# Performance work log

Hardware: AMD Instinct MI355X
Metric: run time of the kernel (lower is better)

The kernel has to match this reference:

```python
import jax, jax.numpy as jnp
import numpy as np

B, C, H, W = 32, 256, 32, 32
C8 = C // 8


def setup_inputs() -> dict:
    key = jax.random.key(0)
    ks = jax.random.split(key, 8)
    s = 1.0 / np.sqrt(C)
    return {
        "x": jax.random.normal(ks[0], (B, C, H, W), dtype=jnp.float32),
        "Wq": jax.random.normal(ks[1], (C8, C), dtype=jnp.float32) * s,
        "bq": jax.random.normal(ks[2], (C8,), dtype=jnp.float32) * s,
        "Wk": jax.random.normal(ks[3], (C8, C), dtype=jnp.float32) * s,
        "bk": jax.random.normal(ks[4], (C8,), dtype=jnp.float32) * s,
        "Wv": jax.random.normal(ks[5], (C, C), dtype=jnp.float32) * s,
        "bv": jax.random.normal(ks[6], (C,), dtype=jnp.float32) * s,
        "gamma": jax.random.normal(ks[7], (1,), dtype=jnp.float32) * 0.1,
    }


def reference(x, Wq, bq, Wk, bk, Wv, bv, gamma):
    b, c, h, w = x.shape
    n = h * w
    xf = x.reshape(b, c, n)  # [B, C, N]
    # 1x1 convs == per-pixel linear projections
    q = jnp.einsum('dc,bcn->bnd', Wq, xf) + bq            # [B, N, C/8]
    k = jnp.einsum('dc,bcn->bdn', Wk, xf) + bk[:, None]    # [B, C/8, N]
    v = jnp.einsum('dc,bcn->bdn', Wv, xf) + bv[:, None]    # [B, C, N]
    energy = jnp.einsum('bnd,bdm->bnm', q, k)              # [B, N, N], no scaling (as in source)
    attn = jax.nn.softmax(energy, axis=-1)                 # softmax over keys
    # out[:, :, i] = sum_j V[:, :, j] * attn[i, j]
    out = jnp.einsum('bdn,bmn->bdm', v, attn)              # [B, C, N]
    out = out.reshape(b, c, h, w)
    return gamma * out + x
```

## Files before the change

kernel.cpp:

```cpp
#include <hip/hip_runtime.h>
#include <math.h>

#define BB 32
#define CC 256
#define CQ 32
#define NN 1024

typedef short bf16x8 __attribute__((ext_vector_type(8)));
typedef float f32x4  __attribute__((ext_vector_type(4)));
typedef unsigned short u16;

__device__ __forceinline__ u16 f2bf(float f) {
    unsigned u = __float_as_uint(f);
    u = (u + 0x7FFFu + ((u >> 16) & 1u)) >> 16;
    return (u16)u;
}

__device__ __forceinline__ unsigned cvt_pk_bf16(float lo, float hi) {
    unsigned r;
    asm("v_cvt_pk_bf16_f32 %0, %1, %2" : "=v"(r) : "v"(lo), "v"(hi));
    return r;
}

__global__ void wpack_kernel(const float* __restrict__ Wq,
                             const float* __restrict__ Wk,
                             const float* __restrict__ Wv,
                             u16* __restrict__ wfrag)
{
    const int o = blockIdx.x * 256 + threadIdx.x;
    const int j    = o & 7;
    const int lane = (o >> 3) & 63;
    const int kc   = (o >> 9) & 7;
    const int rt   = o >> 12;
    const int row  = rt * 16 + (lane & 15);
    const int col  = kc * 32 + (lane >> 4) * 8 + j;
    const float v = (row < 32) ? Wq[row * 256 + col]
                  : (row < 64) ? Wk[(row - 32) * 256 + col]
                               : Wv[(row - 64) * 256 + col];
    wfrag[o] = f2bf(v);
}

struct QSmem {
    union {
        u16 xs[32][268];
        u16 osv[CC][40];
    };
    u16 osqk[32][72];
};

__global__ __launch_bounds__(256, 4) void qkv_kernel(
    const float* __restrict__ x, const u16* __restrict__ wfrag,
    const float* __restrict__ bq, const float* __restrict__ bk,
    const float* __restrict__ bv,
    u16* __restrict__ qt, u16* __restrict__ kt, u16* __restrict__ vv)
{
    __shared__ QSmem sm;
    const int b = blockIdx.y, n0 = blockIdx.x * 32;
    const int t = threadIdx.x;
    const int lane = t & 63, w = t >> 6;
    const int quad = lane >> 4, c16 = lane & 15;

    {
        const float* xb = x + (size_t)b * CC * NN + n0;
        const int n4 = (t & 7) * 4;
        const int cr = t >> 3;
        float4 f[8];
#pragma unroll
        for (int it = 0; it < 8; ++it)
            f[it] = *(const float4*)(xb + (size_t)(it * 32 + cr) * NN + n4);
#pragma unroll
        for (int it = 0; it < 8; ++it) {
            const int c = it * 32 + cr;
            sm.xs[n4 + 0][c] = f2bf(f[it].x);
            sm.xs[n4 + 1][c] = f2bf(f[it].y);
            sm.xs[n4 + 2][c] = f2bf(f[it].z);
            sm.xs[n4 + 3][c] = f2bf(f[it].w);
        }
    }
    __syncthreads();

    f32x4 acc[5][2];
#pragma unroll
    for (int i = 0; i < 5; ++i)
#pragma unroll
        for (int j = 0; j < 2; ++j) acc[i][j] = (f32x4){0.f, 0.f, 0.f, 0.f};

#pragma unroll 2
    for (int k = 0; k < 8; ++k) {
        const int c0 = k * 32;
        bf16x8 wa[5], xb[2];
#pragma unroll
        for (int rs = 0; rs < 5; ++rs)
            wa[rs] = *(const bf16x8*)&wfrag[(size_t)(((w * 5 + rs) * 8 + k) * 64 + lane) * 8];
#pragma unroll
        for (int ns = 0; ns < 2; ++ns) {
            const short4 a = *(const short4*)&sm.xs[ns * 16 + c16][c0 + quad * 8];
            const short4 b2 = *(const short4*)&sm.xs[ns * 16 + c16][c0 + quad * 8 + 4];
            bf16x8 v;
            v[0] = a.x; v[1] = a.y; v[2] = a.z; v[3] = a.w;
            v[4] = b2.x; v[5] = b2.y; v[6] = b2.z; v[7] = b2.w;
            xb[ns] = v;
        }
#pragma unroll
        for (int rs = 0; rs < 5; ++rs)
#pragma unroll
            for (int ns = 0; ns < 2; ++ns)
                acc[rs][ns] = __builtin_amdgcn_mfma_f32_16x16x32_bf16(
                    wa[rs], xb[ns], acc[rs][ns], 0, 0, 0);
    }

    __syncthreads();

#pragma unroll
    for (int rs = 0; rs < 5; ++rs) {
#pragma unroll
        for (int r = 0; r < 4; ++r) {
            const int rg = w * 80 + rs * 16 + quad * 4 + r;
            const float bias = (rg < 32) ? bq[rg] : (rg < 64) ? bk[rg - 32] : bv[rg - 64];
#pragma unroll
            for (int ns = 0; ns < 2; ++ns) {
                const int n = ns * 16 + c16;
                const u16 h = f2bf(acc[rs][ns][r] + bias);
                if (rg < 64) sm.osqk[n][rg] = h;
                else         sm.osv[rg - 64][n] = h;
            }
        }
    }
    __syncthreads();

    {
        u16* dst = (t >= 128) ? kt : qt;
        const int dof = (t >= 128) ? 32 : 0;
        const int o = (t & 127) * 8;
        const int n = o >> 5, d = o & 31;
        const bf16x8 v = *(const bf16x8*)&sm.osqk[n][d + dof];
        *(bf16x8*)&dst[((size_t)b * NN + n0) * CQ + o] = v;
    }
#pragma unroll
    for (int it = 0; it < 4; ++it) {
        const int o = it * 2048 + t * 8;
        const int c = o >> 5, n = o & 31;
        const bf16x8 v = *(const bf16x8*)&sm.osv[c][n];
        *(bf16x8*)&vv[((size_t)b * CC + c) * NN + n0 + n] = v;
    }
}

__global__ __launch_bounds__(512, 4) void attn_kernel(
    const u16* __restrict__ qt, const u16* __restrict__ kt,
    const u16* __restrict__ vv, const float* __restrict__ x,
    const float* __restrict__ gamma_p, float* __restrict__ out)
{
    __shared__ u16 ps16[2][64][136];
    __shared__ float lsh[64];

    const int bid  = blockIdx.x;
    const int xcd  = bid & 7;
    const int slot = bid >> 3;
    const int b    = (xcd << 2) | (slot >> 4);
    const int m0   = (slot & 15) * 64;

    const int t = threadIdx.x, lane = t & 63, w = t >> 6;
    const int quad = lane >> 4, c16 = lane & 15;
    const int ch   = c16 >> 3;
    const int c7   = c16 & 7;
    const int qkey = (c16 >> 2) & 3;
    const int sm   = w & 3;
    const int sh   = w >> 2;
    const int ms0  = w & 3;

    const bf16x8 qa = *(const bf16x8*)&qt[((size_t)b * NN + m0 + sm * 16 + c16) * CQ + quad * 8];

    bf16x8 ones;
#pragma unroll
    for (int j = 0; j < 8; ++j) ones[j] = (short)0x3F80;

    f32x4 accO[2][4];
    f32x4 lsum = (f32x4){0.f, 0.f, 0.f, 0.f};
#pragma unroll
    for (int cs = 0; cs < 2; ++cs)
#pragma unroll
        for (int j = 0; j < 4; ++j) accO[cs][j] = (f32x4){0.f, 0.f, 0.f, 0.f};

    const u16* vbase = vv + (size_t)b * CC * NN;
    const u16* kbase = kt + (size_t)b * NN * CQ;

    bf16x8 kb[4];
#pragma unroll
    for (int s = 0; s < 4; ++s)
        kb[s] = *(const bf16x8*)&kbase[(size_t)(sh * 64 + s * 16 + c16) * CQ + quad * 8];

    for (int step = 0; step < 8; ++step) {
        const int nbase = step * 128;
        u16* psb = &ps16[step & 1][0][0];

        bf16x8 va[2][4];
#pragma unroll
        for (int cs = 0; cs < 2; ++cs)
#pragma unroll
            for (int kc = 0; kc < 4; ++kc)
                va[cs][kc] = *(const bf16x8*)&vbase[
                    (size_t)(w * 32 + cs * 16 + c16) * NN + nbase + kc * 32 + quad * 8];

        f32x4 accS[4];
#pragma unroll
        for (int s = 0; s < 4; ++s)
            accS[s] = __builtin_amdgcn_mfma_f32_16x16x32_bf16(
                qa, kb[s], (f32x4){0.f, 0.f, 0.f, 0.f}, 0, 0, 0);

        const int rowb = sm * 16 + quad * 4;
#pragma unroll
        for (int s = 0; s < 4; ++s) {
            const int nbt = sh * 8 + 2 * s + ch;
            const int p = nbt ^ quad;
            u16* pw = &psb[rowb * 136 + p * 8 + c7];
            const float e0 = __expf(accS[s][0]);
            const float e1 = __expf(accS[s][1]);
            const float e2 = __expf(accS[s][2]);
            const float e3 = __expf(accS[s][3]);
            const unsigned p01 = cvt_pk_bf16(e0, e1);
            const unsigned p23 = cvt_pk_bf16(e2, e3);
            pw[0]   = (u16)p01;
            pw[136] = (u16)(p01 >> 16);
            pw[272] = (u16)p23;
            pw[408] = (u16)(p23 >> 16);
        }

        if (step < 7) {
#pragma unroll
            for (int s = 0; s < 4; ++s)
                kb[s] = *(const bf16x8*)&kbase[
                    (size_t)(nbase + 128 + sh * 64 + s * 16 + c16) * CQ + quad * 8];
        }

        asm volatile("s_waitcnt lgkmcnt(0)" ::: "memory");
        __builtin_amdgcn_s_barrier();
        asm volatile("" ::: "memory");

        __builtin_amdgcn_s_setprio(1);
#pragma unroll
        for (int msi = 0; msi < 4; ++msi) {
            bf16x8 pb[4];
#pragma unroll
            for (int kc = 0; kc < 4; ++kc)
                pb[kc] = *(const bf16x8*)&psb[(msi * 16 + c16) * 136
                                              + (4 * kc + (quad ^ qkey)) * 8];
            if (msi == ms0) {
#pragma unroll
                for (int kc = 0; kc < 4; ++kc)
                    lsum = __builtin_amdgcn_mfma_f32_16x16x32_bf16(ones, pb[kc], lsum, 0, 0, 0);
            }
#pragma unroll
            for (int cs = 0; cs < 2; ++cs)
#pragma unroll
                for (int kc = 0; kc < 4; ++kc)
                    accO[cs][msi] = __builtin_amdgcn_mfma_f32_16x16x32_bf16(
                        va[cs][kc], pb[kc], accO[cs][msi], 0, 0, 0);
        }
        __builtin_amdgcn_s_setprio(0);
    }

    if (sh == 0 && quad == 0) lsh[ms0 * 16 + c16] = lsum[0];
    __syncthreads();

    const float gamma = gamma_p[0];
#pragma unroll
    for (int ms = 0; ms < 4; ++ms) {
        const float inv = gamma / lsh[ms * 16 + c16];
        const int m = m0 + ms * 16 + c16;
#pragma unroll
        for (int cs = 0; cs < 2; ++cs) {
            const int cbase = w * 32 + cs * 16 + quad * 4;
#pragma unroll
            for (int r = 0; r < 4; ++r) {
                const size_t idx = ((size_t)b * CC + cbase + r) * NN + m;
                out[idx] = accO[cs][ms][r] * inv + x[idx];
            }
        }
    }
}

extern "C" void kernel_launch(void* const* d_in, const int* in_sizes, int n_in,
                              void* d_out, int out_size, void* d_ws, size_t ws_size,
                              hipStream_t stream)
{
    const float* x  = (const float*)d_in[0];
    const float* Wq = (const float*)d_in[1];
    const float* bq = (const float*)d_in[2];
    const float* Wk = (const float*)d_in[3];
    const float* bk = (const float*)d_in[4];
    const float* Wv = (const float*)d_in[5];
    const float* bv = (const float*)d_in[6];
    const float* gm = (const float*)d_in[7];
    float* out = (float*)d_out;

    u16* qt    = (u16*)d_ws;
    u16* kt    = qt + (size_t)BB * NN * CQ;
    u16* vv    = kt + (size_t)BB * NN * CQ;
    u16* wfrag = vv + (size_t)BB * CC * NN;

    wpack_kernel<<<320, 256, 0, stream>>>(Wq, Wk, Wv, wfrag);
    dim3 grid(32, BB);
    qkv_kernel<<<grid, 256, 0, stream>>>(x, wfrag, bq, bk, bv, qt, kt, vv);
    attn_kernel<<<512, 512, 0, stream>>>(qt, kt, vv, x, gm, out);
}
```

Baseline: 150.9 us.

## Keep softmax probabilities in registers by permuting K rows, removing LDS staging

The qkv kernel now writes K rows in a permuted order, so that computing S^T = K·Q with MFMA leaves the exp'd probabilities in the exact register layout the PV MFMA needs as its B operand. The attention kernel no longer stages P through shared memory, so the LDS buffers and per-step barriers are gone. Work is also repartitioned: 256-thread blocks, each wave owning 32 query rows × 128 channels and walking keys in 32-wide chunks with double-buffered K loads. The trade-off is fewer waves per block, larger accumulator register pressure (16 accumulators per wave), and V being reloaded per 32-key chunk.

```diff
diff --git a/kernel.cpp b/kernel.cpp
--- a/kernel.cpp
+++ b/kernel.cpp
@@ -129,12 +129,16 @@
     __syncthreads();
 
     {
-        u16* dst = (t >= 128) ? kt : qt;
-        const int dof = (t >= 128) ? 32 : 0;
         const int o = (t & 127) * 8;
         const int n = o >> 5, d = o & 31;
-        const bf16x8 v = *(const bf16x8*)&sm.osqk[n][d + dof];
-        *(bf16x8*)&dst[((size_t)b * NN + n0) * CQ + o] = v;
+        if (t < 128) {
+            const bf16x8 v = *(const bf16x8*)&sm.osqk[n][d];
+            *(bf16x8*)&qt[((size_t)b * NN + n0) * CQ + n * 32 + d] = v;
+        } else {
+            const int p = ((n & 0x18) >> 1) | ((n & 4) << 2) | (n & 3);
+            const bf16x8 v = *(const bf16x8*)&sm.osqk[n][d + 32];
+            *(bf16x8*)&kt[((size_t)b * NN + n0) * CQ + p * 32 + d] = v;
+        }
     }
 #pragma unroll
     for (int it = 0; it < 4; ++it) {
@@ -145,135 +149,97 @@
     }
 }
 
-__global__ __launch_bounds__(512, 4) void attn_kernel(
+__global__ __launch_bounds__(256, 2) void attn_kernel(
     const u16* __restrict__ qt, const u16* __restrict__ kt,
     const u16* __restrict__ vv, const float* __restrict__ x,
     const float* __restrict__ gamma_p, float* __restrict__ out)
 {
-    __shared__ u16 ps16[2][64][136];
-    __shared__ float lsh[64];
-
     const int bid  = blockIdx.x;
     const int xcd  = bid & 7;
     const int slot = bid >> 3;
     const int b    = (xcd << 2) | (slot >> 4);
-    const int m0   = (slot & 15) * 64;
+    const int m0b  = (slot & 15) * 64;
 
     const int t = threadIdx.x, lane = t & 63, w = t >> 6;
     const int quad = lane >> 4, c16 = lane & 15;
-    const int ch   = c16 >> 3;
-    const int c7   = c16 & 7;
-    const int qkey = (c16 >> 2) & 3;
-    const int sm   = w & 3;
-    const int sh   = w >> 2;
-    const int ms0  = w & 3;
-
-    const bf16x8 qa = *(const bf16x8*)&qt[((size_t)b * NN + m0 + sm * 16 + c16) * CQ + quad * 8];
+    const int m0 = m0b + (w & 1) * 32;
+    const int c0 = (w >> 1) * 128;
+
+    bf16x8 qa[2];
+#pragma unroll
+    for (int mt = 0; mt < 2; ++mt)
+        qa[mt] = *(const bf16x8*)&qt[((size_t)b * NN + m0 + mt * 16 + c16) * CQ + quad * 8];
 
     bf16x8 ones;
 #pragma unroll
     for (int j = 0; j < 8; ++j) ones[j] = (short)0x3F80;
 
-    f32x4 accO[2][4];
-    f32x4 lsum = (f32x4){0.f, 0.f, 0.f, 0.f};
-#pragma unroll
-    for (int cs = 0; cs < 2; ++cs)
-#pragma unroll
-        for (int j = 0; j < 4; ++j) accO[cs][j] = (f32x4){0.f, 0.f, 0.f, 0.f};
-
-    const u16* vbase = vv + (size_t)b * CC * NN;
-    const u16* kbase = kt + (size_t)b * NN * CQ;
-
-    bf16x8 kb[4];
-#pragma unroll
-    for (int s = 0; s < 4; ++s)
-        kb[s] = *(const bf16x8*)&kbase[(size_t)(sh * 64 + s * 16 + c16) * CQ + quad * 8];
-
-    for (int step = 0; step < 8; ++step) {
-        const int nbase = step * 128;
-        u16* psb = &ps16[step & 1][0][0];
-
-        bf16x8 va[2][4];
-#pragma unroll
-        for (int cs = 0; cs < 2; ++cs)
-#pragma unroll
-            for (int kc = 0; kc < 4; ++kc)
-                va[cs][kc] = *(const bf16x8*)&vbase[
-                    (size_t)(w * 32 + cs * 16 + c16) * NN + nbase + kc * 32 + quad * 8];
-
-        f32x4 accS[4];
-#pragma unroll
-        for (int s = 0; s < 4; ++s)
-            accS[s] = __builtin_amdgcn_mfma_f32_16x16x32_bf16(
-                qa, kb[s], (f32x4){0.f, 0.f, 0.f, 0.f}, 0, 0, 0);
-
-        const int rowb = sm * 16 + quad * 4;
-#pragma unroll
-        for (int s = 0; s < 4; ++s) {
-            const int nbt = sh * 8 + 2 * s + ch;
-            const int p = nbt ^ quad;
-            u16* pw = &psb[rowb * 136 + p * 8 + c7];
-            const float e0 = __expf(accS[s][0]);
-            const float e1 = __expf(accS[s][1]);
-            const float e2 = __expf(accS[s][2]);
-            const float e3 = __expf(accS[s][3]);
-            const unsigned p01 = cvt_pk_bf16(e0, e1);
-            const unsigned p23 = cvt_pk_bf16(e2, e3);
-            pw[0]   = (u16)p01;
-            pw[136] = (u16)(p01 >> 16);
-            pw[272] = (u16)p23;
-            pw[408] = (u16)(p23 >> 16);
-        }
-
-        if (step < 7) {
-#pragma unroll
-            for (int s = 0; s < 4; ++s)
-                kb[s] = *(const bf16x8*)&kbase[
-                    (size_t)(nbase + 128 + sh * 64 + s * 16 + c16) * CQ + quad * 8];
-        }
-
-        asm volatile("s_waitcnt lgkmcnt(0)" ::: "memory");
-        __builtin_amdgcn_s_barrier();
-        asm volatile("" ::: "memory");
-
-        __builtin_amdgcn_s_setprio(1);
-#pragma unroll
-        for (int msi = 0; msi < 4; ++msi) {
-            bf16x8 pb[4];
-#pragma unroll
-            for (int kc = 0; kc < 4; ++kc)
-                pb[kc] = *(const bf16x8*)&psb[(msi * 16 + c16) * 136
-                                              + (4 * kc + (quad ^ qkey)) * 8];
-            if (msi == ms0) {
-#pragma unroll
-                for (int kc = 0; kc < 4; ++kc)
-                    lsum = __builtin_amdgcn_mfma_f32_16x16x32_bf16(ones, pb[kc], lsum, 0, 0, 0);
-            }
-#pragma unroll
-            for (int cs = 0; cs < 2; ++cs)
-#pragma unroll
-                for (int kc = 0; kc < 4; ++kc)
-                    accO[cs][msi] = __builtin_amdgcn_mfma_f32_16x16x32_bf16(
-                        va[cs][kc], pb[kc], accO[cs][msi], 0, 0, 0);
-        }
-        __builtin_amdgcn_s_setprio(0);
-    }
-
-    if (sh == 0 && quad == 0) lsh[ms0 * 16 + c16] = lsum[0];
-    __syncthreads();
+    f32x4 accO[8][2];
+    f32x4 lsum[2];
+#pragma unroll
+    for (int mt = 0; mt < 2; ++mt) {
+        lsum[mt] = (f32x4){0.f, 0.f, 0.f, 0.f};
+#pragma unroll
+        for (int cs = 0; cs < 8; ++cs) accO[cs][mt] = (f32x4){0.f, 0.f, 0.f, 0.f};
+    }
+
+    const u16* vb = vv + (size_t)b * CC * NN;
+    const u16* kp = kt + (size_t)b * NN * CQ;
+
+    bf16x8 kbA[2], kbB[2];
+#pragma unroll
+    for (int tt = 0; tt < 2; ++tt)
+        kbA[tt] = *(const bf16x8*)&kp[(size_t)(tt * 16 + c16) * CQ + quad * 8];
+
+    auto CHUNK = [&](int cb, bf16x8 (&kbC)[2], bf16x8 (&kbN)[2]) {
+        const int nb = cb * 32;
+        bf16x8 va[8];
+#pragma unroll
+        for (int cs = 0; cs < 8; ++cs)
+            va[cs] = *(const bf16x8*)&vb[(size_t)(c0 + cs * 16 + c16) * NN + nb + quad * 8];
+        if (cb + 1 < 32) {
+#pragma unroll
+            for (int tt = 0; tt < 2; ++tt)
+                kbN[tt] = *(const bf16x8*)&kp[(size_t)(nb + 32 + tt * 16 + c16) * CQ + quad * 8];
+        }
+#pragma unroll
+        for (int mt = 0; mt < 2; ++mt) {
+            f32x4 s0 = __builtin_amdgcn_mfma_f32_16x16x32_bf16(
+                kbC[0], qa[mt], (f32x4){0.f, 0.f, 0.f, 0.f}, 0, 0, 0);
+            f32x4 s1 = __builtin_amdgcn_mfma_f32_16x16x32_bf16(
+                kbC[1], qa[mt], (f32x4){0.f, 0.f, 0.f, 0.f}, 0, 0, 0);
+            union { unsigned u[4]; bf16x8 v; } pu;
+            pu.u[0] = cvt_pk_bf16(__expf(s0[0]), __expf(s0[1]));
+            pu.u[1] = cvt_pk_bf16(__expf(s0[2]), __expf(s0[3]));
+            pu.u[2] = cvt_pk_bf16(__expf(s1[0]), __expf(s1[1]));
+            pu.u[3] = cvt_pk_bf16(__expf(s1[2]), __expf(s1[3]));
+            const bf16x8 pb = pu.v;
+            lsum[mt] = __builtin_amdgcn_mfma_f32_16x16x32_bf16(ones, pb, lsum[mt], 0, 0, 0);
+#pragma unroll
+            for (int cs = 0; cs < 8; ++cs)
+                accO[cs][mt] = __builtin_amdgcn_mfma_f32_16x16x32_bf16(
+                    va[cs], pb, accO[cs][mt], 0, 0, 0);
+        }
+    };
+
+#pragma unroll 1
+    for (int cb = 0; cb < 32; cb += 2) {
+        CHUNK(cb,     kbA, kbB);
+        CHUNK(cb + 1, kbB, kbA);
+    }
 
     const float gamma = gamma_p[0];
 #pragma unroll
-    for (int ms = 0; ms < 4; ++ms) {
-        const float inv = gamma / lsh[ms * 16 + c16];
-        const int m = m0 + ms * 16 + c16;
-#pragma unroll
-        for (int cs = 0; cs < 2; ++cs) {
-            const int cbase = w * 32 + cs * 16 + quad * 4;
+    for (int mt = 0; mt < 2; ++mt) {
+        const float inv = gamma / lsum[mt][0];
+        const int m = m0 + mt * 16 + c16;
+#pragma unroll
+        for (int cs = 0; cs < 8; ++cs) {
+            const int cb2 = c0 + cs * 16 + quad * 4;
 #pragma unroll
             for (int r = 0; r < 4; ++r) {
-                const size_t idx = ((size_t)b * CC + cbase + r) * NN + m;
-                out[idx] = accO[cs][ms][r] * inv + x[idx];
+                const size_t idx = ((size_t)b * CC + cb2 + r) * NN + m;
+                out[idx] = accO[cs][mt][r] * inv + x[idx];
             }
         }
     }
@@ -301,5 +267,5 @@
     wpack_kernel<<<320, 256, 0, stream>>>(Wq, Wk, Wv, wfrag);
     dim3 grid(32, BB);
     qkv_kernel<<<grid, 256, 0, stream>>>(x, wfrag, bq, bk, bv, qt, kt, vv);
-    attn_kernel<<<512, 512, 0, stream>>>(qt, kt, vv, x, gm, out);
-}
+    attn_kernel<<<512, 256, 0, stream>>>(qt, kt, vv, x, gm, out);
+}
```

After: 180.2 us. 19.4% more time.

## Retile attention PV loop into 2x4 warp grid with 64-key steps

Applied to the files above, without the earlier changes.

Changes the warp decomposition of the P·V product from each warp owning 32 channels across all 64 query rows to each warp owning 64 channels across 32 query rows. The key step size is halved from 128 to 64, so there are 16 iterations with a smaller shared P buffer. Each warp now reads only half of the P tile from LDS per step, which cuts LDS read traffic and register pressure from V fragments. The cost is twice as many barriers, the s_setprio hints are removed, and each V fragment is now loaded by two warps, doubling global/L2 V traffic.

```diff
diff --git a/kernel.cpp b/kernel.cpp
--- a/kernel.cpp
+++ b/kernel.cpp
@@ -150,7 +150,7 @@
     const u16* __restrict__ vv, const float* __restrict__ x,
     const float* __restrict__ gamma_p, float* __restrict__ out)
 {
-    __shared__ u16 ps16[2][64][136];
+    __shared__ u16 ps16[2][64][72];
     __shared__ float lsh[64];
 
     const int bid  = blockIdx.x;
@@ -164,9 +164,11 @@
     const int ch   = c16 >> 3;
     const int c7   = c16 & 7;
     const int qkey = (c16 >> 2) & 3;
-    const int sm   = w & 3;
-    const int sh   = w >> 2;
-    const int ms0  = w & 3;
+    const int mh   = w & 1;
+    const int cq   = w >> 1;
+    const int sm   = mh * 2 + (cq & 1);
+    const int sh   = cq >> 1;
+    const int c0   = cq * 64;
 
     const bf16x8 qa = *(const bf16x8*)&qt[((size_t)b * NN + m0 + sm * 16 + c16) * CQ + quad * 8];
 
@@ -174,45 +176,46 @@
 #pragma unroll
     for (int j = 0; j < 8; ++j) ones[j] = (short)0x3F80;
 
-    f32x4 accO[2][4];
-    f32x4 lsum = (f32x4){0.f, 0.f, 0.f, 0.f};
-#pragma unroll
-    for (int cs = 0; cs < 2; ++cs)
-#pragma unroll
-        for (int j = 0; j < 4; ++j) accO[cs][j] = (f32x4){0.f, 0.f, 0.f, 0.f};
+    f32x4 accO[4][2];
+    f32x4 lsum[2];
+#pragma unroll
+    for (int mi = 0; mi < 2; ++mi) {
+        lsum[mi] = (f32x4){0.f, 0.f, 0.f, 0.f};
+#pragma unroll
+        for (int cs = 0; cs < 4; ++cs) accO[cs][mi] = (f32x4){0.f, 0.f, 0.f, 0.f};
+    }
 
     const u16* vbase = vv + (size_t)b * CC * NN;
     const u16* kbase = kt + (size_t)b * NN * CQ;
 
-    bf16x8 kb[4];
-#pragma unroll
-    for (int s = 0; s < 4; ++s)
-        kb[s] = *(const bf16x8*)&kbase[(size_t)(sh * 64 + s * 16 + c16) * CQ + quad * 8];
-
-    for (int step = 0; step < 8; ++step) {
-        const int nbase = step * 128;
+    bf16x8 kb[2];
+#pragma unroll
+    for (int s = 0; s < 2; ++s)
+        kb[s] = *(const bf16x8*)&kbase[(size_t)(sh * 32 + s * 16 + c16) * CQ + quad * 8];
+
+    for (int step = 0; step < 16; ++step) {
+        const int nbase = step * 64;
         u16* psb = &ps16[step & 1][0][0];
 
-        bf16x8 va[2][4];
-#pragma unroll
-        for (int cs = 0; cs < 2; ++cs)
-#pragma unroll
-            for (int kc = 0; kc < 4; ++kc)
+        bf16x8 va[4][2];
+#pragma unroll
+        for (int cs = 0; cs < 4; ++cs)
+#pragma unroll
+            for (int kc = 0; kc < 2; ++kc)
                 va[cs][kc] = *(const bf16x8*)&vbase[
-                    (size_t)(w * 32 + cs * 16 + c16) * NN + nbase + kc * 32 + quad * 8];
-
-        f32x4 accS[4];
-#pragma unroll
-        for (int s = 0; s < 4; ++s)
+                    (size_t)(c0 + cs * 16 + c16) * NN + nbase + kc * 32 + quad * 8];
+
+        f32x4 accS[2];
+#pragma unroll
+        for (int s = 0; s < 2; ++s)
             accS[s] = __builtin_amdgcn_mfma_f32_16x16x32_bf16(
                 qa, kb[s], (f32x4){0.f, 0.f, 0.f, 0.f}, 0, 0, 0);
 
         const int rowb = sm * 16 + quad * 4;
 #pragma unroll
-        for (int s = 0; s < 4; ++s) {
-            const int nbt = sh * 8 + 2 * s + ch;
-            const int p = nbt ^ quad;
-            u16* pw = &psb[rowb * 136 + p * 8 + c7];
+        for (int s = 0; s < 2; ++s) {
+            const int nb = (sh * 4 + 2 * s + ch) ^ quad;
+            u16* pw = &psb[rowb * 72 + nb * 8 + c7];
             const float e0 = __expf(accS[s][0]);
             const float e1 = __expf(accS[s][1]);
             const float e2 = __expf(accS[s][2]);
@@ -220,60 +223,60 @@
             const unsigned p01 = cvt_pk_bf16(e0, e1);
             const unsigned p23 = cvt_pk_bf16(e2, e3);
             pw[0]   = (u16)p01;
-            pw[136] = (u16)(p01 >> 16);
-            pw[272] = (u16)p23;
-            pw[408] = (u16)(p23 >> 16);
-        }
-
-        if (step < 7) {
-#pragma unroll
-            for (int s = 0; s < 4; ++s)
+            pw[72]  = (u16)(p01 >> 16);
+            pw[144] = (u16)p23;
+            pw[216] = (u16)(p23 >> 16);
+        }
+
+        if (step < 15) {
+#pragma unroll
+            for (int s = 0; s < 2; ++s)
                 kb[s] = *(const bf16x8*)&kbase[
-                    (size_t)(nbase + 128 + sh * 64 + s * 16 + c16) * CQ + quad * 8];
-        }
-
-        asm volatile("s_waitcnt lgkmcnt(0)" ::: "memory");
-        __builtin_amdgcn_s_barrier();
-        asm volatile("" ::: "memory");
-
-        __builtin_amdgcn_s_setprio(1);
-#pragma unroll
-        for (int msi = 0; msi < 4; ++msi) {
-            bf16x8 pb[4];
-#pragma unroll
-            for (int kc = 0; kc < 4; ++kc)
-                pb[kc] = *(const bf16x8*)&psb[(msi * 16 + c16) * 136
+                    (size_t)(nbase + 64 + sh * 32 + s * 16 + c16) * CQ + quad * 8];
+        }
+
+        __syncthreads();
+
+#pragma unroll
+        for (int mi = 0; mi < 2; ++mi) {
+            const int msi = mh * 2 + mi;
+            bf16x8 pb[2];
+#pragma unroll
+            for (int kc = 0; kc < 2; ++kc)
+                pb[kc] = *(const bf16x8*)&psb[(msi * 16 + c16) * 72
                                               + (4 * kc + (quad ^ qkey)) * 8];
-            if (msi == ms0) {
-#pragma unroll
-                for (int kc = 0; kc < 4; ++kc)
-                    lsum = __builtin_amdgcn_mfma_f32_16x16x32_bf16(ones, pb[kc], lsum, 0, 0, 0);
+            if (cq == 0) {
+                lsum[mi] = __builtin_amdgcn_mfma_f32_16x16x32_bf16(ones, pb[0], lsum[mi], 0, 0, 0);
+                lsum[mi] = __builtin_amdgcn_mfma_f32_16x16x32_bf16(ones, pb[1], lsum[mi], 0, 0, 0);
             }
 #pragma unroll
-            for (int cs = 0; cs < 2; ++cs)
-#pragma unroll
-                for (int kc = 0; kc < 4; ++kc)
-                    accO[cs][msi] = __builtin_amdgcn_mfma_f32_16x16x32_bf16(
-                        va[cs][kc], pb[kc], accO[cs][msi], 0, 0, 0);
-        }
-        __builtin_amdgcn_s_setprio(0);
-    }
-
-    if (sh == 0 && quad == 0) lsh[ms0 * 16 + c16] = lsum[0];
+            for (int cs = 0; cs < 4; ++cs)
+#pragma unroll
+                for (int kc = 0; kc < 2; ++kc)
+                    accO[cs][mi] = __builtin_amdgcn_mfma_f32_16x16x32_bf16(
+                        va[cs][kc], pb[kc], accO[cs][mi], 0, 0, 0);
+        }
+    }
+
+    if (cq == 0 && quad == 0) {
+        lsh[(mh * 2 + 0) * 16 + c16] = lsum[0][0];
+        lsh[(mh * 2 + 1) * 16 + c16] = lsum[1][0];
+    }
     __syncthreads();
 
     const float gamma = gamma_p[0];
 #pragma unroll
-    for (int ms = 0; ms < 4; ++ms) {
-        const float inv = gamma / lsh[ms * 16 + c16];
-        const int m = m0 + ms * 16 + c16;
-#pragma unroll
-        for (int cs = 0; cs < 2; ++cs) {
-            const int cbase = w * 32 + cs * 16 + quad * 4;
+    for (int mi = 0; mi < 2; ++mi) {
+        const int msi = mh * 2 + mi;
+        const float inv = gamma / lsh[msi * 16 + c16];
+        const int m = m0 + msi * 16 + c16;
+#pragma unroll
+        for (int cs = 0; cs < 4; ++cs) {
+            const int cbase = c0 + cs * 16 + quad * 4;
 #pragma unroll
             for (int r = 0; r < 4; ++r) {
                 const size_t idx = ((size_t)b * CC + cbase + r) * NN + m;
-                out[idx] = accO[cs][ms][r] * inv + x[idx];
+                out[idx] = accO[cs][mi][r] * inv + x[idx];
             }
         }
     }
```

Measured after the change: 178.1 us. 1.18x slower.
